# Kernel optimization log

Hardware: AMD Instinct MI355X
Metric: run time of the kernel (lower is better)

Reference implementation:

```python
import jax, jax.numpy as jnp
import numpy as np

NEG_SLOPE = 0.2  # PyG GATConv default negative_slope
EPS = 1e-16     # PyG softmax denominator epsilon


def gat_conv(x, src, dst, W, a_src, a_dst, bias):
    """PyG GATConv (concat=True, dropout off). x:[N,Fin], src/dst:[E]."""
    N = x.shape[0]
    H, C = a_src.shape
    h = (x @ W).reshape(N, H, C)                      # per-head projected features
    es = jnp.einsum('nhc,hc->nh', h, a_src)           # alpha_src per node/head
    ed = jnp.einsum('nhc,hc->nh', h, a_dst)           # alpha_dst per node/head
    e = jax.nn.leaky_relu(es[src] + ed[dst], NEG_SLOPE)   # [E,H] edge scores
    # segment softmax over destination nodes (every node has a self loop)
    m = jax.ops.segment_max(e, dst, num_segments=N)
    p = jnp.exp(e - m[dst])
    denom = jax.ops.segment_sum(p, dst, num_segments=N)
    alpha = p / (denom[dst] + EPS)                    # [E,H]
    out = jax.ops.segment_sum(h[src] * alpha[:, :, None], dst, num_segments=N)
    return out.reshape(N, H * C) + bias


def _single_graph(x, ei, W1, a_src1, a_dst1, b1, W2, a_src2, a_dst2, b2):
    N = x.shape[0]
    loop = jnp.arange(N, dtype=ei.dtype)              # add_self_loops=True
    src = jnp.concatenate([ei[0], loop])
    dst = jnp.concatenate([ei[1], loop])
    h = jax.nn.relu(gat_conv(x, src, dst, W1, a_src1, a_dst1, b1))
    # F.dropout with p=0.0 is identity
    return gat_conv(h, src, dst, W2, a_src2, a_dst2, b2)


def setup_inputs() -> dict:
    key = jax.random.key(0)
    ks = jax.random.split(key, 9)
    B, N, E, F_in, H, C = 2, 20000, 320000, 128, 8, 64

    def glorot(k, shape):
        fan_in, fan_out = shape[-2] if len(shape) > 1 else shape[-1], shape[-1]
        s = np.sqrt(6.0 / (fan_in + fan_out)).astype(np.float32)
        return jax.random.uniform(k, shape, jnp.float32, -s, s)

    return {
        'xs': jax.random.normal(ks[0], (B, N, F_in), jnp.float32),
        'edge_indexs': jax.random.randint(ks[1], (B, 2, E), 0, N, jnp.int32),
        'W1': glorot(ks[2], (F_in, H * C)),
        'a_src1': glorot(ks[3], (H, C)),
        'a_dst1': glorot(ks[4], (H, C)),
        'b1': jnp.zeros((H * C,), jnp.float32),
        'W2': glorot(ks[5], (H * C, C)),
        'a_src2': glorot(ks[6], (1, C)),
        'a_dst2': glorot(ks[7], (1, C)),
        'b2': jnp.zeros((C,), jnp.float32),
    }


def reference(xs, edge_indexs, W1, a_src1, a_dst1, b1, W2, a_src2, a_dst2, b2):
    f = lambda x, ei: _single_graph(x, ei, W1, a_src1, a_dst1, b1, W2, a_src2, a_dst2, b2)
    return jax.vmap(f)(xs, edge_indexs)               # [B, N, C]
```

## Files before the change

kernel.cpp:

```cpp
#include <hip/hip_runtime.h>
#include <hip/hip_bf16.h>
#include <cstdint>

#define NEG_SLOPE 0.2f
#define SOFTMAX_EPS 1e-16f
#define NN 20000
#define EE 320000
#define CAP 48

typedef __hip_bfloat16 bf16;
typedef unsigned short ushort;
typedef short s8v __attribute__((ext_vector_type(8)));
typedef float f4v __attribute__((ext_vector_type(4)));

static __device__ __forceinline__ float lo16(unsigned u) { return __uint_as_float(u << 16); }
static __device__ __forceinline__ float hi16(unsigned u) { return __uint_as_float(u & 0xffff0000u); }
static __device__ __forceinline__ ushort f2bf(float v) {
    bf16 h = __float2bfloat16(v);
    return *(ushort*)&h;
}

__global__ void prep_kernel(const float* __restrict__ W1, const float* __restrict__ W2,
                            ushort* __restrict__ w1hi, ushort* __restrict__ w1lo,
                            ushort* __restrict__ w2hi, ushort* __restrict__ w2lo,
                            int* __restrict__ count, ushort* __restrict__ esrc) {
    int bid = blockIdx.x;
    int t = threadIdx.x;
    if (bid >= 48) {
        int idx = (bid - 48) * 256 + t;
        if (idx < 2 * NN) {
            count[idx] = 1;
            esrc[(size_t)idx * CAP] = (ushort)(idx % NN);
        }
        return;
    }
    __shared__ float T[32][65];
    const float* src; ushort *dhi, *dlo; int K, C, c0, k0;
    if (bid < 32) { src = W1; dhi = w1hi; dlo = w1lo; K = 128; C = 512; c0 = (bid & 7) * 64; k0 = (bid >> 3) * 32; }
    else          { src = W2; dhi = w2hi; dlo = w2lo; K = 512; C = 64;  c0 = 0;              k0 = (bid - 32) * 32; }
    for (int i = 0; i < 8; ++i) {
        int flat = t + i * 256;
        int k = flat >> 6, c = flat & 63;
        T[k][c] = src[(size_t)(k0 + k) * C + c0 + c];
    }
    __syncthreads();
    int c = t >> 2, j0 = (t & 3) * 8;
    unsigned hp[4], lp[4];
#pragma unroll
    for (int p = 0; p < 4; ++p) {
        float v0 = T[j0 + p * 2][c], v1 = T[j0 + p * 2 + 1][c];
        ushort h0 = f2bf(v0), h1 = f2bf(v1);
        float l0 = v0 - __uint_as_float((unsigned)h0 << 16);
        float l1 = v1 - __uint_as_float((unsigned)h1 << 16);
        hp[p] = (unsigned)h0 | ((unsigned)h1 << 16);
        lp[p] = (unsigned)f2bf(l0) | ((unsigned)f2bf(l1) << 16);
    }
    size_t o = (size_t)(c0 + c) * K + k0 + j0;
    *(uint4*)&dhi[o] = make_uint4(hp[0], hp[1], hp[2], hp[3]);
    *(uint4*)&dlo[o] = make_uint4(lp[0], lp[1], lp[2], lp[3]);
}

__global__ void scatter_bucket(const int* __restrict__ ei, int* __restrict__ count,
                               ushort* __restrict__ esrc) {
    int e = blockIdx.x * blockDim.x + threadIdx.x;
    if (e >= EE) return;
    int b = blockIdx.y;
    const int* srcA = ei + (size_t)b * 2 * EE;
    int s = srcA[e], d = srcA[EE + e];
    if ((unsigned)d >= NN || (unsigned)s >= NN) return;
    int pos = atomicAdd(&count[b * NN + d], 1);
    if (pos < CAP)
        esrc[((size_t)b * NN + d) * CAP + pos] = (ushort)s;
}

#define G1S 40
__global__ __launch_bounds__(256) void gemm1_mfma(
        const float* __restrict__ xs, const ushort* __restrict__ w1hi,
        const ushort* __restrict__ w1lo, const float* __restrict__ a_src,
        const float* __restrict__ a_dst, bf16* __restrict__ h1,
        float* __restrict__ es, float* __restrict__ ed) {
    __shared__ ushort lds[25600];
    ushort* Xhi = lds;
    ushort* Xlo = lds + 2560;
    ushort* Whi = lds + 5120;
    ushort* Wlo = lds + 15360;

    int t = threadIdx.x;
    int w = t >> 6, lane = t & 63, quad = lane >> 4, l16 = lane & 15;
    int nhalf = blockIdx.y, b = blockIdx.z;
    int row0 = blockIdx.x * 64, nbase = nhalf * 256;
    const float* x = xs + (size_t)b * NN * 128;
    bf16*  h1b = h1 + (size_t)b * NN * 512;
    float* esb = es + (size_t)b * NN * 8;
    float* edb = ed + (size_t)b * NN * 8;

    f4v acc[16];
#pragma unroll
    for (int i = 0; i < 16; ++i) acc[i] = (f4v)0.f;

    for (int kc = 0; kc < 4; ++kc) {
        __syncthreads();
        {
            int row = t >> 2, c0 = (t & 3) * 8;
            float v[8];
            if (row0 + row < NN) {
                float4 A = *(const float4*)&x[(size_t)(row0 + row) * 128 + kc * 32 + c0];
                float4 B = *(const float4*)&x[(size_t)(row0 + row) * 128 + kc * 32 + c0 + 4];
                v[0] = A.x; v[1] = A.y; v[2] = A.z; v[3] = A.w;
                v[4] = B.x; v[5] = B.y; v[6] = B.z; v[7] = B.w;
            } else {
#pragma unroll
                for (int i = 0; i < 8; ++i) v[i] = 0.f;
            }
            unsigned hp[4], lp[4];
#pragma unroll
            for (int p = 0; p < 4; ++p) {
                ushort h0 = f2bf(v[p * 2]), h1_ = f2bf(v[p * 2 + 1]);
                float l0 = v[p * 2] - __uint_as_float((unsigned)h0 << 16);
                float l1 = v[p * 2 + 1] - __uint_as_float((unsigned)h1_ << 16);
                hp[p] = (unsigned)h0 | ((unsigned)h1_ << 16);
                lp[p] = (unsigned)f2bf(l0) | ((unsigned)f2bf(l1) << 16);
            }
            *(uint4*)&Xhi[row * G1S + c0] = make_uint4(hp[0], hp[1], hp[2], hp[3]);
            *(uint4*)&Xlo[row * G1S + c0] = make_uint4(lp[0], lp[1], lp[2], lp[3]);
        }
        {
            const ushort* sh = w1hi + (size_t)(nbase + t) * 128 + kc * 32;
            const ushort* sl = w1lo + (size_t)(nbase + t) * 128 + kc * 32;
            uint4 h0 = *(const uint4*)(sh), h1_ = *(const uint4*)(sh + 8);
            uint4 h2 = *(const uint4*)(sh + 16), h3 = *(const uint4*)(sh + 24);
            uint4 l0 = *(const uint4*)(sl), l1 = *(const uint4*)(sl + 8);
            uint4 l2 = *(const uint4*)(sl + 16), l3 = *(const uint4*)(sl + 24);
            *(uint4*)&Whi[t * G1S]      = h0; *(uint4*)&Whi[t * G1S + 8]  = h1_;
            *(uint4*)&Whi[t * G1S + 16] = h2; *(uint4*)&Whi[t * G1S + 24] = h3;
            *(uint4*)&Wlo[t * G1S]      = l0; *(uint4*)&Wlo[t * G1S + 8]  = l1;
            *(uint4*)&Wlo[t * G1S + 16] = l2; *(uint4*)&Wlo[t * G1S + 24] = l3;
        }
        __syncthreads();
        int arow = (w * 16 + l16) * G1S + quad * 8;
        s8v ahi = *(const s8v*)&Xhi[arow];
        s8v alo = *(const s8v*)&Xlo[arow];
#pragma unroll
        for (int ct = 0; ct < 16; ++ct) {
            int baddr = (ct * 16 + l16) * G1S + quad * 8;
            s8v bhi = *(const s8v*)&Whi[baddr];
            s8v blo = *(const s8v*)&Wlo[baddr];
            acc[ct] = __builtin_amdgcn_mfma_f32_16x16x32_bf16(ahi, bhi, acc[ct], 0, 0, 0);
            acc[ct] = __builtin_amdgcn_mfma_f32_16x16x32_bf16(ahi, blo, acc[ct], 0, 0, 0);
            acc[ct] = __builtin_amdgcn_mfma_f32_16x16x32_bf16(alo, bhi, acc[ct], 0, 0, 0);
        }
    }

#pragma unroll
    for (int hh = 0; hh < 4; ++hh) {
        float s4[4] = {0.f, 0.f, 0.f, 0.f}, d4[4] = {0.f, 0.f, 0.f, 0.f};
#pragma unroll
        for (int ct4 = 0; ct4 < 4; ++ct4) {
            int ct = hh * 4 + ct4;
            int c = nbase + ct * 16 + l16;
            float as = a_src[c], ad = a_dst[c];
#pragma unroll
            for (int r = 0; r < 4; ++r) { s4[r] += acc[ct][r] * as; d4[r] += acc[ct][r] * ad; }
        }
#pragma unroll
        for (int o = 1; o < 16; o <<= 1) {
#pragma unroll
            for (int r = 0; r < 4; ++r) {
                s4[r] += __shfl_xor(s4[r], o);
                d4[r] += __shfl_xor(d4[r], o);
            }
        }
        if (l16 == 0) {
            int head = nhalf * 4 + hh;
#pragma unroll
            for (int r = 0; r < 4; ++r) {
                int gr = row0 + w * 16 + quad * 4 + r;
                if (gr < NN) { esb[gr * 8 + head] = s4[r]; edb[gr * 8 + head] = d4[r]; }
            }
        }
    }

    __syncthreads();
    ushort* rp = lds + w * 4224;
#pragma unroll
    for (int ct = 0; ct < 16; ++ct)
#pragma unroll
        for (int r = 0; r < 4; ++r)
            rp[(quad * 4 + r) * 264 + ct * 16 + l16] = f2bf(acc[ct][r]);
#pragma unroll
    for (int i = 0; i < 8; ++i) {
        int idx = i * 512 + lane * 8;
        int row = idx >> 8, col = idx & 255;
        uint4 vv = *(const uint4*)&rp[row * 264 + col];
        int gr = row0 + w * 16 + row;
        if (gr < NN) *(uint4*)&h1b[(size_t)gr * 512 + nbase + col] = vv;
    }
}

#define G2S 72
__global__ __launch_bounds__(256) void gemm2_mfma(
        const bf16* __restrict__ a, const ushort* __restrict__ w2hi,
        const ushort* __restrict__ w2lo, const float* __restrict__ a_src,
        const float* __restrict__ a_dst, bf16* __restrict__ h2,
        float* __restrict__ es, float* __restrict__ ed) {
    __shared__ ushort lds[13824];
    ushort* AS  = lds;
    ushort* Whi = lds + 4608;
    ushort* Wlo = lds + 9216;

    int t = threadIdx.x;
    int w = t >> 6, lane = t & 63, quad = lane >> 4, l16 = lane & 15;
    int b = blockIdx.y;
    int row0 = blockIdx.x * 64;
    const bf16* ab = a + (size_t)b * NN * 512;
    bf16*  h2b = h2 + (size_t)b * NN * 64;
    float* esb = es + (size_t)b * NN;
    float* edb = ed + (size_t)b * NN;

    f4v acc[4];
#pragma unroll
    for (int i = 0; i < 4; ++i) acc[i] = (f4v)0.f;

    for (int kc = 0; kc < 8; ++kc) {
        __syncthreads();
        {
            int row = t >> 2, k0 = (t & 3) * 16;
            uint4 q0, q1;
            if (row0 + row < NN) {
                q0 = *(const uint4*)(ab + (size_t)(row0 + row) * 512 + kc * 64 + k0);
                q1 = *(const uint4*)(ab + (size_t)(row0 + row) * 512 + kc * 64 + k0 + 8);
            } else { q0 = make_uint4(0, 0, 0, 0); q1 = q0; }
            *(uint4*)&AS[row * G2S + k0]     = q0;
            *(uint4*)&AS[row * G2S + k0 + 8] = q1;
            const ushort* sh = w2hi + (size_t)row * 512 + kc * 64 + k0;
            const ushort* sl = w2lo + (size_t)row * 512 + kc * 64 + k0;
            *(uint4*)&Whi[row * G2S + k0]     = *(const uint4*)(sh);
            *(uint4*)&Whi[row * G2S + k0 + 8] = *(const uint4*)(sh + 8);
            *(uint4*)&Wlo[row * G2S + k0]     = *(const uint4*)(sl);
            *(uint4*)&Wlo[row * G2S + k0 + 8] = *(const uint4*)(sl + 8);
        }
        __syncthreads();
#pragma unroll
        for (int ks = 0; ks < 2; ++ks) {
            s8v av = *(const s8v*)&AS[(w * 16 + l16) * G2S + ks * 32 + quad * 8];
#pragma unroll
            for (int ct = 0; ct < 4; ++ct) {
                int baddr = (ct * 16 + l16) * G2S + ks * 32 + quad * 8;
                s8v bhi = *(const s8v*)&Whi[baddr];
                s8v blo = *(const s8v*)&Wlo[baddr];
                acc[ct] = __builtin_amdgcn_mfma_f32_16x16x32_bf16(av, bhi, acc[ct], 0, 0, 0);
                acc[ct] = __builtin_amdgcn_mfma_f32_16x16x32_bf16(av, blo, acc[ct], 0, 0, 0);
            }
        }
    }

    {
        float s4[4] = {0.f, 0.f, 0.f, 0.f}, d4[4] = {0.f, 0.f, 0.f, 0.f};
#pragma unroll
        for (int ct = 0; ct < 4; ++ct) {
            int c = ct * 16 + l16;
            float as = a_src[c], ad = a_dst[c];
#pragma unroll
            for (int r = 0; r < 4; ++r) { s4[r] += acc[ct][r] * as; d4[r] += acc[ct][r] * ad; }
        }
#pragma unroll
        for (int o = 1; o < 16; o <<= 1) {
#pragma unroll
            for (int r = 0; r < 4; ++r) {
                s4[r] += __shfl_xor(s4[r], o);
                d4[r] += __shfl_xor(d4[r], o);
            }
        }
        if (l16 == 0) {
#pragma unroll
            for (int r = 0; r < 4; ++r) {
                int gr = row0 + w * 16 + quad * 4 + r;
                if (gr < NN) { esb[gr] = s4[r]; edb[gr] = d4[r]; }
            }
        }
    }

    __syncthreads();
    ushort* rp = lds + w * 1152;
#pragma unroll
    for (int ct = 0; ct < 4; ++ct)
#pragma unroll
        for (int r = 0; r < 4; ++r)
            rp[(quad * 4 + r) * G2S + ct * 16 + l16] = f2bf(acc[ct][r]);
#pragma unroll
    for (int i = 0; i < 2; ++i) {
        int idx = i * 512 + lane * 8;
        int row = idx >> 6, col = idx & 63;
        uint4 vv = *(const uint4*)&rp[row * G2S + col];
        int gr = row0 + w * 16 + row;
        if (gr < NN) *(uint4*)&h2b[(size_t)gr * 64 + col] = vv;
    }
}

__global__ __launch_bounds__(256) void aggregate1_kernel(
        const bf16* __restrict__ h1, const float* __restrict__ es,
        const float* __restrict__ ed, const int* __restrict__ count,
        const ushort* __restrict__ esrc, const float* __restrict__ b1,
        bf16* __restrict__ out1) {
    __shared__ float alds[4][8][68];
    int b = blockIdx.y;
    const bf16*  h1b = h1 + (size_t)b * NN * 512;
    const float* esb = es + (size_t)b * NN * 8;
    const float* edb = ed + (size_t)b * NN * 8;
    bf16* out1b = out1 + (size_t)b * NN * 512;

    int t = threadIdx.x;
    int wv = t >> 6, lane = t & 63;
    int n = blockIdx.x * 4 + wv;
    int deg = count[b * NN + n];
    deg = max(0, min(deg, CAP));
    size_t beg = ((size_t)b * NN + n) * CAP;

    float4 ed0 = *(const float4*)&edb[n * 8];
    float4 ed1 = *(const float4*)&edb[n * 8 + 4];
    float edh[8] = {ed0.x, ed0.y, ed0.z, ed0.w, ed1.x, ed1.y, ed1.z, ed1.w};

    int myhead = lane >> 3;
    float acc[8];
#pragma unroll
    for (int i = 0; i < 8; ++i) acc[i] = 0.f;

    bool act = lane < deg;
    int sreg = act ? (int)esrc[beg + lane] : 0;
    float4 s0 = *(const float4*)&esb[(size_t)sreg * 8];
    float4 s1 = *(const float4*)&esb[(size_t)sreg * 8 + 4];
    float e[8] = {s0.x, s0.y, s0.z, s0.w, s1.x, s1.y, s1.z, s1.w};
    float m[8], p[8], sum[8];
#pragma unroll
    for (int h = 0; h < 8; ++h) {
        float v = e[h] + edh[h];
        v = (v >= 0.f) ? v : NEG_SLOPE * v;
        e[h] = act ? v : -1e30f;
        m[h] = e[h];
    }
#pragma unroll
    for (int o = 32; o > 0; o >>= 1) {
#pragma unroll
        for (int h = 0; h < 8; ++h) m[h] = fmaxf(m[h], __shfl_xor(m[h], o));
    }
#pragma unroll
    for (int h = 0; h < 8; ++h) { p[h] = act ? __expf(e[h] - m[h]) : 0.f; sum[h] = p[h]; }
#pragma unroll
    for (int o = 32; o > 0; o >>= 1) {
#pragma unroll
        for (int h = 0; h < 8; ++h) sum[h] += __shfl_xor(sum[h], o);
    }
#pragma unroll
    for (int h = 0; h < 8; ++h)
        alds[wv][h][lane] = p[h] / (sum[h] + SOFTMAX_EPS);

    int j = 0;
    for (; j + 3 < deg; j += 4) {
        int sa = __shfl(sreg, j),     sb = __shfl(sreg, j + 1);
        int sc = __shfl(sreg, j + 2), sd = __shfl(sreg, j + 3);
        float wa = alds[wv][myhead][j],     wb = alds[wv][myhead][j + 1];
        float wc = alds[wv][myhead][j + 2], wd = alds[wv][myhead][j + 3];
        uint4 ua = *(const uint4*)(h1b + (size_t)sa * 512 + lane * 8);
        uint4 ub = *(const uint4*)(h1b + (size_t)sb * 512 + lane * 8);
        uint4 uc = *(const uint4*)(h1b + (size_t)sc * 512 + lane * 8);
        uint4 ud = *(const uint4*)(h1b + (size_t)sd * 512 + lane * 8);
        acc[0] += wa * lo16(ua.x); acc[1] += wa * hi16(ua.x);
        acc[2] += wa * lo16(ua.y); acc[3] += wa * hi16(ua.y);
        acc[4] += wa * lo16(ua.z); acc[5] += wa * hi16(ua.z);
        acc[6] += wa * lo16(ua.w); acc[7] += wa * hi16(ua.w);
        acc[0] += wb * lo16(ub.x); acc[1] += wb * hi16(ub.x);
        acc[2] += wb * lo16(ub.y); acc[3] += wb * hi16(ub.y);
        acc[4] += wb * lo16(ub.z); acc[5] += wb * hi16(ub.z);
        acc[6] += wb * lo16(ub.w); acc[7] += wb * hi16(ub.w);
        acc[0] += wc * lo16(uc.x); acc[1] += wc * hi16(uc.x);
        acc[2] += wc * lo16(uc.y); acc[3] += wc * hi16(uc.y);
        acc[4] += wc * lo16(uc.z); acc[5] += wc * hi16(uc.z);
        acc[6] += wc * lo16(uc.w); acc[7] += wc * hi16(uc.w);
        acc[0] += wd * lo16(ud.x); acc[1] += wd * hi16(ud.x);
        acc[2] += wd * lo16(ud.y); acc[3] += wd * hi16(ud.y);
        acc[4] += wd * lo16(ud.z); acc[5] += wd * hi16(ud.z);
        acc[6] += wd * lo16(ud.w); acc[7] += wd * hi16(ud.w);
    }
    for (; j < deg; ++j) {
        int sa = __shfl(sreg, j);
        float wa = alds[wv][myhead][j];
        uint4 ua = *(const uint4*)(h1b + (size_t)sa * 512 + lane * 8);
        acc[0] += wa * lo16(ua.x); acc[1] += wa * hi16(ua.x);
        acc[2] += wa * lo16(ua.y); acc[3] += wa * hi16(ua.y);
        acc[4] += wa * lo16(ua.z); acc[5] += wa * hi16(ua.z);
        acc[6] += wa * lo16(ua.w); acc[7] += wa * hi16(ua.w);
    }

    float4 bv0 = *(const float4*)&b1[lane * 8];
    float4 bv1 = *(const float4*)&b1[lane * 8 + 4];
    float bias[8] = {bv0.x, bv0.y, bv0.z, bv0.w, bv1.x, bv1.y, bv1.z, bv1.w};
    union { ushort us[8]; uint4 u4; } pack;
#pragma unroll
    for (int i = 0; i < 8; ++i)
        pack.us[i] = f2bf(fmaxf(acc[i] + bias[i], 0.f));
    *(uint4*)(out1b + (size_t)n * 512 + lane * 8) = pack.u4;
}

__global__ void aggregate2_kernel(const bf16* __restrict__ h2, const float* __restrict__ es,
                                  const float* __restrict__ ed, const int* __restrict__ count,
                                  const ushort* __restrict__ esrc, const float* __restrict__ bias2,
                                  float* __restrict__ out) {
    __shared__ float wl[4][64];
    __shared__ int slidx[4][64];
    int b = blockIdx.y;
    const bf16*  h2b = h2 + (size_t)b * NN * 64;
    const float* esb = es + (size_t)b * NN;
    const float* edb = ed + (size_t)b * NN;
    float* outb = out + (size_t)b * NN * 64;

    int t = threadIdx.x;
    int wv = t >> 6, lane = t & 63;
    int n = blockIdx.x * 4 + wv;
    int deg = count[b * NN + n];
    deg = max(0, min(deg, CAP));
    size_t beg = ((size_t)b * NN + n) * CAP;
    float edn = edb[n];

    bool act = lane < deg;
    int sreg = act ? (int)esrc[beg + lane] : 0;
    float ev = act ? esb[sreg] + edn : -1e30f;
    ev = (ev >= 0.f) ? ev : NEG_SLOPE * ev;
    if (!act) ev = -1e30f;
    float m = ev;
#pragma unroll
    for (int o = 32; o > 0; o >>= 1) m = fmaxf(m, __shfl_xor(m, o));
    float p = act ? __expf(ev - m) : 0.f;
    float sum = p;
#pragma unroll
    for (int o = 32; o > 0; o >>= 1) sum += __shfl_xor(sum, o);
    slidx[wv][lane] = sreg;
    wl[wv][lane] = p / (sum + SOFTMAX_EPS);

    float acc[4] = {0.f, 0.f, 0.f, 0.f};
    int grp = lane >> 4, ch4 = (lane & 15) * 4;
    for (int j = grp; j < deg; j += 4) {
        int s = slidx[wv][j];
        float wt = wl[wv][j];
        uint2 u = *(const uint2*)(h2b + (size_t)s * 64 + ch4);
        acc[0] += wt * lo16(u.x); acc[1] += wt * hi16(u.x);
        acc[2] += wt * lo16(u.y); acc[3] += wt * hi16(u.y);
    }
#pragma unroll
    for (int i = 0; i < 4; ++i) {
        acc[i] += __shfl_xor(acc[i], 16);
        acc[i] += __shfl_xor(acc[i], 32);
    }
    if (lane < 16) {
        float4 o4;
        o4.x = acc[0] + bias2[ch4 + 0];
        o4.y = acc[1] + bias2[ch4 + 1];
        o4.z = acc[2] + bias2[ch4 + 2];
        o4.w = acc[3] + bias2[ch4 + 3];
        *(float4*)&outb[(size_t)n * 64 + ch4] = o4;
    }
}

extern "C" void kernel_launch(void* const* d_in, const int* in_sizes, int n_in,
                              void* d_out, int out_size, void* d_ws, size_t ws_size,
                              hipStream_t stream) {
    const float* xs     = (const float*)d_in[0];
    const int*   ei     = (const int*)d_in[1];
    const float* W1     = (const float*)d_in[2];
    const float* a_src1 = (const float*)d_in[3];
    const float* a_dst1 = (const float*)d_in[4];
    const float* b1     = (const float*)d_in[5];
    const float* W2     = (const float*)d_in[6];
    const float* a_src2 = (const float*)d_in[7];
    const float* a_dst2 = (const float*)d_in[8];
    const float* b2     = (const float*)d_in[9];
    float* out = (float*)d_out;

    const int B = 2;

    uintptr_t p = (uintptr_t)d_ws;
    auto alloc = [&](size_t bytes) {
        void* r = (void*)p;
        p += (bytes + 255) & ~(size_t)255;
        return r;
    };
    bf16* h1   = (bf16*)alloc((size_t)B * NN * 512 * 2);
    bf16* out1 = (bf16*)alloc((size_t)B * NN * 512 * 2);
    char* unionA = (char*)alloc((size_t)B * NN * 64 * 2);
    float*  es1   = (float*)unionA;
    float*  ed1   = (float*)(unionA + 1280000);
    ushort* wt1hi = (ushort*)(unionA + 2560000);
    ushort* wt1lo = (ushort*)(unionA + 2560000 + 131072);
    bf16*   h2    = (bf16*)unionA;
    ushort* wt2hi = (ushort*)alloc((size_t)64 * 512 * 2);
    ushort* wt2lo = (ushort*)alloc((size_t)64 * 512 * 2);
    float* es2    = (float*)alloc((size_t)B * NN * 4);
    float* ed2    = (float*)alloc((size_t)B * NN * 4);
    int*   count  = (int*)alloc((size_t)B * NN * 4);
    ushort* esrc  = (ushort*)alloc((size_t)B * NN * CAP * 2);

    const int initBlocks = (2 * NN + 255) / 256;
    prep_kernel<<<48 + initBlocks, 256, 0, stream>>>(W1, W2, wt1hi, wt1lo, wt2hi, wt2lo,
                                                     count, esrc);
    scatter_bucket<<<dim3((EE + 255) / 256, B), 256, 0, stream>>>(ei, count, esrc);
    gemm1_mfma<<<dim3(313, 2, 2), 256, 0, stream>>>(xs, wt1hi, wt1lo, a_src1, a_dst1, h1, es1, ed1);
    aggregate1_kernel<<<dim3(NN / 4, B), 256, 0, stream>>>(h1, es1, ed1, count, esrc, b1, out1);
    gemm2_mfma<<<dim3(313, B), 256, 0, stream>>>(out1, wt2hi, wt2lo, a_src2, a_dst2, h2, es2, ed2);
    aggregate2_kernel<<<dim3(NN / 4, B), 256, 0, stream>>>(h2, es2, ed2, count, esrc, b2, out);
}
```

Baseline: 285.8 us.

## Fuse edge bucketing into GEMM1 launch and read W1 directly from global

Merges the scatter_bucket kernel into the gemm1 launch as extra blocks, so one kernel launch is removed and the scatter work can run alongside the GEMM. GEMM1 now stages all of X (full K) in LDS once with a single barrier, and each lane reads its W1 fragments directly from global/L2 instead of through LDS. This drops the per-k-chunk syncs and shrinks LDS use, at the cost of more redundant global reads of W1 across waves. It also unrolls the aggregate2 gather loop by two so that two loads are in flight at once.

Measured after the change: 330.5 us. +15.7%, slower.

```diff
diff --git a/kernel.cpp b/kernel.cpp
--- a/kernel.cpp
+++ b/kernel.cpp
@@ -60,52 +60,54 @@
     *(uint4*)&dlo[o] = make_uint4(lp[0], lp[1], lp[2], lp[3]);
 }
 
-__global__ void scatter_bucket(const int* __restrict__ ei, int* __restrict__ count,
-                               ushort* __restrict__ esrc) {
-    int e = blockIdx.x * blockDim.x + threadIdx.x;
-    if (e >= EE) return;
-    int b = blockIdx.y;
-    const int* srcA = ei + (size_t)b * 2 * EE;
-    int s = srcA[e], d = srcA[EE + e];
-    if ((unsigned)d >= NN || (unsigned)s >= NN) return;
-    int pos = atomicAdd(&count[b * NN + d], 1);
-    if (pos < CAP)
-        esrc[((size_t)b * NN + d) * CAP + pos] = (ushort)s;
-}
-
-#define G1S 40
-__global__ __launch_bounds__(256) void gemm1_mfma(
+#define XS 136
+#define GEMM1_BLOCKS 1252
+__global__ __launch_bounds__(256) void gemm1_scatter(
         const float* __restrict__ xs, const ushort* __restrict__ w1hi,
         const ushort* __restrict__ w1lo, const float* __restrict__ a_src,
         const float* __restrict__ a_dst, bf16* __restrict__ h1,
-        float* __restrict__ es, float* __restrict__ ed) {
-    __shared__ ushort lds[25600];
+        float* __restrict__ es, float* __restrict__ ed,
+        const int* __restrict__ ei, int* __restrict__ count,
+        ushort* __restrict__ esrc) {
+    __shared__ ushort lds[17408];
+    int t = threadIdx.x;
+    int bid = blockIdx.x;
+
+    if (bid >= GEMM1_BLOCKS) {
+        int idx = bid - GEMM1_BLOCKS;
+        int b = idx / 1250;
+        int e = (idx % 1250) * 256 + t;
+        const int* srcA = ei + (size_t)b * 2 * EE;
+        int s = srcA[e], d = srcA[EE + e];
+        if ((unsigned)d >= NN || (unsigned)s >= NN) return;
+        int pos = atomicAdd(&count[b * NN + d], 1);
+        if (pos < CAP)
+            esrc[((size_t)b * NN + d) * CAP + pos] = (ushort)s;
+        return;
+    }
+
     ushort* Xhi = lds;
-    ushort* Xlo = lds + 2560;
-    ushort* Whi = lds + 5120;
-    ushort* Wlo = lds + 15360;
-
-    int t = threadIdx.x;
+    ushort* Xlo = lds + 8704;
     int w = t >> 6, lane = t & 63, quad = lane >> 4, l16 = lane & 15;
-    int nhalf = blockIdx.y, b = blockIdx.z;
-    int row0 = blockIdx.x * 64, nbase = nhalf * 256;
+    int b = bid / 626;
+    int rem = bid % 626;
+    int nhalf = rem / 313;
+    int row0 = (rem % 313) * 64, nbase = nhalf * 256;
     const float* x = xs + (size_t)b * NN * 128;
     bf16*  h1b = h1 + (size_t)b * NN * 512;
     float* esb = es + (size_t)b * NN * 8;
     float* edb = ed + (size_t)b * NN * 8;
 
-    f4v acc[16];
-#pragma unroll
-    for (int i = 0; i < 16; ++i) acc[i] = (f4v)0.f;
-
-    for (int kc = 0; kc < 4; ++kc) {
-        __syncthreads();
-        {
-            int row = t >> 2, c0 = (t & 3) * 8;
+    {
+        int row = t >> 2, k0 = (t & 3) * 32;
+        bool inb = (row0 + row) < NN;
+        const float* xr = x + (size_t)(row0 + row) * 128 + k0;
+#pragma unroll
+        for (int p = 0; p < 4; ++p) {
             float v[8];
-            if (row0 + row < NN) {
-                float4 A = *(const float4*)&x[(size_t)(row0 + row) * 128 + kc * 32 + c0];
-                float4 B = *(const float4*)&x[(size_t)(row0 + row) * 128 + kc * 32 + c0 + 4];
+            if (inb) {
+                float4 A = *(const float4*)(xr + p * 8);
+                float4 B = *(const float4*)(xr + p * 8 + 4);
                 v[0] = A.x; v[1] = A.y; v[2] = A.z; v[3] = A.w;
                 v[4] = B.x; v[5] = B.y; v[6] = B.z; v[7] = B.w;
             } else {
@@ -114,37 +116,33 @@
             }
             unsigned hp[4], lp[4];
 #pragma unroll
-            for (int p = 0; p < 4; ++p) {
-                ushort h0 = f2bf(v[p * 2]), h1_ = f2bf(v[p * 2 + 1]);
-                float l0 = v[p * 2] - __uint_as_float((unsigned)h0 << 16);
-                float l1 = v[p * 2 + 1] - __uint_as_float((unsigned)h1_ << 16);
-                hp[p] = (unsigned)h0 | ((unsigned)h1_ << 16);
-                lp[p] = (unsigned)f2bf(l0) | ((unsigned)f2bf(l1) << 16);
-            }
-            *(uint4*)&Xhi[row * G1S + c0] = make_uint4(hp[0], hp[1], hp[2], hp[3]);
-            *(uint4*)&Xlo[row * G1S + c0] = make_uint4(lp[0], lp[1], lp[2], lp[3]);
-        }
-        {
-            const ushort* sh = w1hi + (size_t)(nbase + t) * 128 + kc * 32;
-            const ushort* sl = w1lo + (size_t)(nbase + t) * 128 + kc * 32;
-            uint4 h0 = *(const uint4*)(sh), h1_ = *(const uint4*)(sh + 8);
-            uint4 h2 = *(const uint4*)(sh + 16), h3 = *(const uint4*)(sh + 24);
-            uint4 l0 = *(const uint4*)(sl), l1 = *(const uint4*)(sl + 8);
-            uint4 l2 = *(const uint4*)(sl + 16), l3 = *(const uint4*)(sl + 24);
-            *(uint4*)&Whi[t * G1S]      = h0; *(uint4*)&Whi[t * G1S + 8]  = h1_;
-            *(uint4*)&Whi[t * G1S + 16] = h2; *(uint4*)&Whi[t * G1S + 24] = h3;
-            *(uint4*)&Wlo[t * G1S]      = l0; *(uint4*)&Wlo[t * G1S + 8]  = l1;
-            *(uint4*)&Wlo[t * G1S + 16] = l2; *(uint4*)&Wlo[t * G1S + 24] = l3;
-        }
-        __syncthreads();
-        int arow = (w * 16 + l16) * G1S + quad * 8;
+            for (int q = 0; q < 4; ++q) {
+                ushort h0 = f2bf(v[q * 2]), h1_ = f2bf(v[q * 2 + 1]);
+                float l0 = v[q * 2] - __uint_as_float((unsigned)h0 << 16);
+                float l1 = v[q * 2 + 1] - __uint_as_float((unsigned)h1_ << 16);
+                hp[q] = (unsigned)h0 | ((unsigned)h1_ << 16);
+                lp[q] = (unsigned)f2bf(l0) | ((unsigned)f2bf(l1) << 16);
+            }
+            *(uint4*)&Xhi[row * XS + k0 + p * 8] = make_uint4(hp[0], hp[1], hp[2], hp[3]);
+            *(uint4*)&Xlo[row * XS + k0 + p * 8] = make_uint4(lp[0], lp[1], lp[2], lp[3]);
+        }
+    }
+    __syncthreads();
+
+    f4v acc[16];
+#pragma unroll
+    for (int i = 0; i < 16; ++i) acc[i] = (f4v)0.f;
+
+#pragma unroll
+    for (int kc = 0; kc < 4; ++kc) {
+        int arow = (w * 16 + l16) * XS + kc * 32 + quad * 8;
         s8v ahi = *(const s8v*)&Xhi[arow];
         s8v alo = *(const s8v*)&Xlo[arow];
+        size_t woff = (size_t)(nbase + l16) * 128 + kc * 32 + quad * 8;
 #pragma unroll
         for (int ct = 0; ct < 16; ++ct) {
-            int baddr = (ct * 16 + l16) * G1S + quad * 8;
-            s8v bhi = *(const s8v*)&Whi[baddr];
-            s8v blo = *(const s8v*)&Wlo[baddr];
+            s8v bhi = *(const s8v*)(w1hi + woff + (size_t)ct * 16 * 128);
+            s8v blo = *(const s8v*)(w1lo + woff + (size_t)ct * 16 * 128);
             acc[ct] = __builtin_amdgcn_mfma_f32_16x16x32_bf16(ahi, bhi, acc[ct], 0, 0, 0);
             acc[ct] = __builtin_amdgcn_mfma_f32_16x16x32_bf16(ahi, blo, acc[ct], 0, 0, 0);
             acc[ct] = __builtin_amdgcn_mfma_f32_16x16x32_bf16(alo, bhi, acc[ct], 0, 0, 0);
@@ -438,7 +436,18 @@
 
     float acc[4] = {0.f, 0.f, 0.f, 0.f};
     int grp = lane >> 4, ch4 = (lane & 15) * 4;
-    for (int j = grp; j < deg; j += 4) {
+    int j = grp;
+    for (; j + 4 < deg; j += 8) {
+        int sA = slidx[wv][j];     float wA = wl[wv][j];
+        int sB = slidx[wv][j + 4]; float wB = wl[wv][j + 4];
+        uint2 uA = *(const uint2*)(h2b + (size_t)sA * 64 + ch4);
+        uint2 uB = *(const uint2*)(h2b + (size_t)sB * 64 + ch4);
+        acc[0] += wA * lo16(uA.x); acc[1] += wA * hi16(uA.x);
+        acc[2] += wA * lo16(uA.y); acc[3] += wA * hi16(uA.y);
+        acc[0] += wB * lo16(uB.x); acc[1] += wB * hi16(uB.x);
+        acc[2] += wB * lo16(uB.y); acc[3] += wB * hi16(uB.y);
+    }
+    for (; j < deg; j += 4) {
         int s = slidx[wv][j];
         float wt = wl[wv][j];
         uint2 u = *(const uint2*)(h2b + (size_t)s * 64 + ch4);
@@ -501,8 +510,8 @@
     const int initBlocks = (2 * NN + 255) / 256;
     prep_kernel<<<48 + initBlocks, 256, 0, stream>>>(W1, W2, wt1hi, wt1lo, wt2hi, wt2lo,
                                                      count, esrc);
-    scatter_bucket<<<dim3((EE + 255) / 256, B), 256, 0, stream>>>(ei, count, esrc);
-    gemm1_mfma<<<dim3(313, 2, 2), 256, 0, stream>>>(xs, wt1hi, wt1lo, a_src1, a_dst1, h1, es1, ed1);
+    gemm1_scatter<<<GEMM1_BLOCKS + 2500, 256, 0, stream>>>(xs, wt1hi, wt1lo, a_src1, a_dst1,
+                                                           h1, es1, ed1, ei, count, esrc);
     aggregate1_kernel<<<dim3(NN / 4, B), 256, 0, stream>>>(h1, es1, ed1, count, esrc, b1, out1);
     gemm2_mfma<<<dim3(313, B), 256, 0, stream>>>(out1, wt2hi, wt2lo, a_src2, a_dst2, h2, es2, ed2);
     aggregate2_kernel<<<dim3(NN / 4, B), 256, 0, stream>>>(h2, es2, ed2, count, esrc, b2, out);
```

## Fuse edge bucketing into GEMM1 launch and synthesize self loops at aggregation

Applied to the files above, without the earlier changes.

The edge scatter/bucketing kernel is merged into the GEMM1 launch as extra trailing blocks, so it runs concurrently with the projection instead of as a separate serialized launch. Self loops are no longer written into the bucket lists. The aggregation kernels instead add one implicit self-loop entry pointing at the node itself. Count initialisation moves to a memset, and the aggregate2 gather loop is unrolled by two to keep more loads in flight. The scatter blocks use LDS-sized blocks, which may reduce co-residency, and the count semantics change, so the per-node cap now applies only to real edges.

New measurement: 275.5 us. -3.6%, faster.

```diff
diff --git a/kernel.cpp b/kernel.cpp
--- a/kernel.cpp
+++ b/kernel.cpp
@@ -22,22 +22,13 @@
 
 __global__ void prep_kernel(const float* __restrict__ W1, const float* __restrict__ W2,
                             ushort* __restrict__ w1hi, ushort* __restrict__ w1lo,
-                            ushort* __restrict__ w2hi, ushort* __restrict__ w2lo,
-                            int* __restrict__ count, ushort* __restrict__ esrc) {
+                            ushort* __restrict__ w2hi, ushort* __restrict__ w2lo) {
+    __shared__ float T[32][65];
     int bid = blockIdx.x;
-    int t = threadIdx.x;
-    if (bid >= 48) {
-        int idx = (bid - 48) * 256 + t;
-        if (idx < 2 * NN) {
-            count[idx] = 1;
-            esrc[(size_t)idx * CAP] = (ushort)(idx % NN);
-        }
-        return;
-    }
-    __shared__ float T[32][65];
     const float* src; ushort *dhi, *dlo; int K, C, c0, k0;
     if (bid < 32) { src = W1; dhi = w1hi; dlo = w1lo; K = 128; C = 512; c0 = (bid & 7) * 64; k0 = (bid >> 3) * 32; }
     else          { src = W2; dhi = w2hi; dlo = w2lo; K = 512; C = 64;  c0 = 0;              k0 = (bid - 32) * 32; }
+    int t = threadIdx.x;
     for (int i = 0; i < 8; ++i) {
         int flat = t + i * 256;
         int k = flat >> 6, c = flat & 63;
@@ -60,35 +51,41 @@
     *(uint4*)&dlo[o] = make_uint4(lp[0], lp[1], lp[2], lp[3]);
 }
 
-__global__ void scatter_bucket(const int* __restrict__ ei, int* __restrict__ count,
-                               ushort* __restrict__ esrc) {
-    int e = blockIdx.x * blockDim.x + threadIdx.x;
-    if (e >= EE) return;
-    int b = blockIdx.y;
-    const int* srcA = ei + (size_t)b * 2 * EE;
-    int s = srcA[e], d = srcA[EE + e];
-    if ((unsigned)d >= NN || (unsigned)s >= NN) return;
-    int pos = atomicAdd(&count[b * NN + d], 1);
-    if (pos < CAP)
-        esrc[((size_t)b * NN + d) * CAP + pos] = (ushort)s;
-}
-
 #define G1S 40
-__global__ __launch_bounds__(256) void gemm1_mfma(
+#define GEMM1_BLOCKS 1252
+__global__ __launch_bounds__(256) void gemm1_scatter(
         const float* __restrict__ xs, const ushort* __restrict__ w1hi,
         const ushort* __restrict__ w1lo, const float* __restrict__ a_src,
         const float* __restrict__ a_dst, bf16* __restrict__ h1,
-        float* __restrict__ es, float* __restrict__ ed) {
+        float* __restrict__ es, float* __restrict__ ed,
+        const int* __restrict__ ei, int* __restrict__ count,
+        ushort* __restrict__ esrc) {
     __shared__ ushort lds[25600];
+    int t = threadIdx.x;
+    int bid = blockIdx.x;
+
+    if (bid >= GEMM1_BLOCKS) {
+        int idx = bid - GEMM1_BLOCKS;
+        int b = idx / 1250;
+        int e = (idx % 1250) * 256 + t;
+        const int* srcA = ei + (size_t)b * 2 * EE;
+        int s = srcA[e], d = srcA[EE + e];
+        if ((unsigned)d >= NN || (unsigned)s >= NN) return;
+        int pos = atomicAdd(&count[b * NN + d], 1);
+        if (pos < CAP)
+            esrc[((size_t)b * NN + d) * CAP + pos] = (ushort)s;
+        return;
+    }
+
     ushort* Xhi = lds;
     ushort* Xlo = lds + 2560;
     ushort* Whi = lds + 5120;
     ushort* Wlo = lds + 15360;
-
-    int t = threadIdx.x;
     int w = t >> 6, lane = t & 63, quad = lane >> 4, l16 = lane & 15;
-    int nhalf = blockIdx.y, b = blockIdx.z;
-    int row0 = blockIdx.x * 64, nbase = nhalf * 256;
+    int b = bid / 626;
+    int rem = bid % 626;
+    int nhalf = rem / 313;
+    int row0 = (rem % 313) * 64, nbase = nhalf * 256;
     const float* x = xs + (size_t)b * NN * 128;
     bf16*  h1b = h1 + (size_t)b * NN * 512;
     float* esb = es + (size_t)b * NN * 8;
@@ -312,8 +309,9 @@
     int t = threadIdx.x;
     int wv = t >> 6, lane = t & 63;
     int n = blockIdx.x * 4 + wv;
-    int deg = count[b * NN + n];
-    deg = max(0, min(deg, CAP));
+    int deg_e = count[b * NN + n];
+    deg_e = max(0, min(deg_e, CAP));
+    int deg = deg_e + 1;
     size_t beg = ((size_t)b * NN + n) * CAP;
 
     float4 ed0 = *(const float4*)&edb[n * 8];
@@ -326,7 +324,7 @@
     for (int i = 0; i < 8; ++i) acc[i] = 0.f;
 
     bool act = lane < deg;
-    int sreg = act ? (int)esrc[beg + lane] : 0;
+    int sreg = act ? ((lane < deg_e) ? (int)esrc[beg + lane] : n) : 0;
     float4 s0 = *(const float4*)&esb[(size_t)sreg * 8];
     float4 s1 = *(const float4*)&esb[(size_t)sreg * 8 + 4];
     float e[8] = {s0.x, s0.y, s0.z, s0.w, s1.x, s1.y, s1.z, s1.w};
@@ -416,13 +414,14 @@
     int t = threadIdx.x;
     int wv = t >> 6, lane = t & 63;
     int n = blockIdx.x * 4 + wv;
-    int deg = count[b * NN + n];
-    deg = max(0, min(deg, CAP));
+    int deg_e = count[b * NN + n];
+    deg_e = max(0, min(deg_e, CAP));
+    int deg = deg_e + 1;
     size_t beg = ((size_t)b * NN + n) * CAP;
     float edn = edb[n];
 
     bool act = lane < deg;
-    int sreg = act ? (int)esrc[beg + lane] : 0;
+    int sreg = act ? ((lane < deg_e) ? (int)esrc[beg + lane] : n) : 0;
     float ev = act ? esb[sreg] + edn : -1e30f;
     ev = (ev >= 0.f) ? ev : NEG_SLOPE * ev;
     if (!act) ev = -1e30f;
@@ -438,7 +437,18 @@
 
     float acc[4] = {0.f, 0.f, 0.f, 0.f};
     int grp = lane >> 4, ch4 = (lane & 15) * 4;
-    for (int j = grp; j < deg; j += 4) {
+    int j = grp;
+    for (; j + 4 < deg; j += 8) {
+        int sA = slidx[wv][j];     float wA = wl[wv][j];
+        int sB = slidx[wv][j + 4]; float wB = wl[wv][j + 4];
+        uint2 uA = *(const uint2*)(h2b + (size_t)sA * 64 + ch4);
+        uint2 uB = *(const uint2*)(h2b + (size_t)sB * 64 + ch4);
+        acc[0] += wA * lo16(uA.x); acc[1] += wA * hi16(uA.x);
+        acc[2] += wA * lo16(uA.y); acc[3] += wA * hi16(uA.y);
+        acc[0] += wB * lo16(uB.x); acc[1] += wB * hi16(uB.x);
+        acc[2] += wB * lo16(uB.y); acc[3] += wB * hi16(uB.y);
+    }
+    for (; j < deg; j += 4) {
         int s = slidx[wv][j];
         float wt = wl[wv][j];
         uint2 u = *(const uint2*)(h2b + (size_t)s * 64 + ch4);
@@ -498,11 +508,10 @@
     int*   count  = (int*)alloc((size_t)B * NN * 4);
     ushort* esrc  = (ushort*)alloc((size_t)B * NN * CAP * 2);
 
-    const int initBlocks = (2 * NN + 255) / 256;
-    prep_kernel<<<48 + initBlocks, 256, 0, stream>>>(W1, W2, wt1hi, wt1lo, wt2hi, wt2lo,
-                                                     count, esrc);
-    scatter_bucket<<<dim3((EE + 255) / 256, B), 256, 0, stream>>>(ei, count, esrc);
-    gemm1_mfma<<<dim3(313, 2, 2), 256, 0, stream>>>(xs, wt1hi, wt1lo, a_src1, a_dst1, h1, es1, ed1);
+    hipMemsetAsync(count, 0, (size_t)B * NN * 4, stream);
+    prep_kernel<<<48, 256, 0, stream>>>(W1, W2, wt1hi, wt1lo, wt2hi, wt2lo);
+    gemm1_scatter<<<GEMM1_BLOCKS + 2500, 256, 0, stream>>>(xs, wt1hi, wt1lo, a_src1, a_dst1,
+                                                           h1, es1, ed1, ei, count, esrc);
     aggregate1_kernel<<<dim3(NN / 4, B), 256, 0, stream>>>(h1, es1, ed1, count, esrc, b1, out1);
     gemm2_mfma<<<dim3(313, B), 256, 0, stream>>>(out1, wt2hi, wt2lo, a_src2, a_dst2, h2, es2, ed2);
     aggregate2_kernel<<<dim3(NN / 4, B), 256, 0, stream>>>(h2, es2, ed2, count, esrc, b2, out);
```
